# Performance work log

Hardware: AMD Instinct MI355X
Metric: run time of the kernel (lower is better)

## Reference

```python
import jax, jax.numpy as jnp
import numpy as np


def setup_inputs() -> dict:
    key = jax.random.key(0)
    kq, kk, kv, km = jax.random.split(key, 4)
    B, H, N, D = 2, 16, 2048, 64
    q = jax.random.normal(kq, (B, H, N, D), dtype=jnp.float32)
    k = jax.random.normal(kk, (B, H, N, D), dtype=jnp.float32)
    v = jax.random.normal(kv, (B, H, N, D), dtype=jnp.float32)
    # mask > 0 means position is masked OUT (matches torch masked_fill(mask > 0, -max))
    mask = jax.random.randint(km, (B, N), 0, 2, dtype=jnp.int32)
    return {"q": q, "k": k, "v": v, "mask": mask}


def reference(q, k, v, mask):
    # q,k,v: [b,h,n,d]; mask: [b,j] with >0 = masked
    scale = q.shape[-1] ** -0.5
    sim = jnp.einsum('bhid,bhjd->bhij', q, k) * scale
    # l2_dist score modification: 2*qk*scale - ||q||^2 - ||k||^2
    q_sq = jnp.sum(q * q, axis=-1, keepdims=True)          # [b,h,i,1]
    k_sq = jnp.sum(k * k, axis=-1, keepdims=True)          # [b,h,j,1]
    sim = sim * 2 - q_sq - jnp.swapaxes(k_sq, -1, -2)       # [b,h,i,j]
    neg_max = -jnp.finfo(sim.dtype).max
    m = (mask > 0)[:, None, None, :]                        # [b,1,1,j]
    sim = jnp.where(m, neg_max, sim)
    attn = jax.nn.softmax(sim, axis=-1)
    out = jnp.einsum('bhij,bhjd->bhid', attn, v)
    return out
```

## Files before the change

### kernel.cpp

```cpp
#include <hip/hip_runtime.h>
#include <hip/hip_bf16.h>

#define NSEQ 2048
#define DD   64
#define HH   16
#define QT   128
#define KVB  64
#define NKV  (NSEQ / KVB)

typedef __attribute__((ext_vector_type(4)))  float f4;
typedef __attribute__((ext_vector_type(16))) float f32x16;
typedef __attribute__((ext_vector_type(8)))  short bf16x8;
typedef __attribute__((ext_vector_type(4)))  unsigned int u32x4;
typedef __attribute__((ext_vector_type(2)))  unsigned int u32x2;

#define QSCL  0.36067376022224085f
#define LOG2E 1.4426950408889634f
#define NEGBIG (-1.0e30f)
#define THR   8.0f

#define SWZ(row, q)  (((row) << 6) + ((((q) ^ ((row) & 7))) << 3))
#define SWZV(d, q)   (((d) << 6) + ((((q) ^ (((d) >> 2) & 7) ^ ((d) & 3))) << 3))

#if defined(__has_builtin)
#if __has_builtin(__builtin_amdgcn_exp2f)
#define EXP2F __builtin_amdgcn_exp2f
#endif
#if __has_builtin(__builtin_amdgcn_permlane32_swap)
#define HAVE_PLSWAP 1
#endif
#endif
#ifndef EXP2F
#define EXP2F exp2f
#endif

union bfu { u32x4 u; bf16x8 h; };

__device__ __forceinline__ unsigned cvtpk(float lo, float hi) {
    unsigned r;
    asm("v_cvt_pk_bf16_f32 %0, %1, %2" : "=v"(r) : "v"(lo), "v"(hi));
    return r;
}
template<int CTRL>
__device__ __forceinline__ float dppf(float x) {
    return __int_as_float(__builtin_amdgcn_update_dpp(
        0, __float_as_int(x), CTRL, 0xF, 0xF, true));
}
__device__ __forceinline__ float cross_max(float x) {
#ifdef HAVE_PLSWAP
    u32x2 r = __builtin_amdgcn_permlane32_swap(__float_as_uint(x), __float_as_uint(x),
                                               false, false);
    return fmaxf(__uint_as_float(r[0]), __uint_as_float(r[1]));
#else
    return fmaxf(x, __shfl_xor(x, 32));
#endif
}
__device__ __forceinline__ float cross_add(float x) {
#ifdef HAVE_PLSWAP
    u32x2 r = __builtin_amdgcn_permlane32_swap(__float_as_uint(x), __float_as_uint(x),
                                               false, false);
    return __uint_as_float(r[0]) + __uint_as_float(r[1]);
#else
    return x + __shfl_xor(x, 32);
#endif
}

__global__ __launch_bounds__(256, 2)
void attend_kernel(const float* __restrict__ qg, const float* __restrict__ kg,
                   const float* __restrict__ vg, const int* __restrict__ maskg,
                   float* __restrict__ outg)
{
    __shared__ __align__(16) unsigned short Ks[2][KVB * DD];
    __shared__ __align__(16) unsigned short Vt[2][DD * KVB];
    __shared__ __align__(16) float bias_s[2][KVB];

    const int t    = threadIdx.x;
    const int w    = t >> 6;
    const int lane = t & 63;
    const int c5   = lane & 31;
    const int g2   = lane >> 5;

    const int p     = blockIdx.x;
    const int bh    = (p & 7) * 4 + ((p >> 3) >> 4);
    const int qtile = (p >> 3) & 15;
    const int b     = bh >> 4;

    const size_t base = (size_t)bh * NSEQ * DD;
    const float* kp = kg + base;
    const float* vp = vg + base;
    const int*   mp = maskg + b * NSEQ;

    bfu qf[4];
    {
        const float* qp = qg + base + (size_t)(qtile*QT + w*32 + c5) * DD;
        #pragma unroll
        for (int ck = 0; ck < 4; ++ck) {
            f4 a  = *(const f4*)(qp + ck*16 + g2*8);
            f4 bb = *(const f4*)(qp + ck*16 + g2*8 + 4);
            qf[ck].u = (u32x4){ cvtpk(a[0]*QSCL,  a[1]*QSCL),  cvtpk(a[2]*QSCL,  a[3]*QSCL),
                                cvtpk(bb[0]*QSCL, bb[1]*QSCL), cvtpk(bb[2]*QSCL, bb[3]*QSCL) };
        }
    }

    f32x16 acc0, acc1;
    #pragma unroll
    for (int r = 0; r < 16; ++r) { acc0[r] = 0.f; acc1[r] = 0.f; }
    float m_run = NEGBIG, l_run = 0.f;

    const bool isK = (w < 2);
    const int  jK  = t >> 1;
    const int  kq0 = (t & 1) * 4;
    const int  uv  = t & 127;
    const int  dq  = uv & 15;
    const int  jq  = uv >> 4;

    f4  st[8];
    int mr = 0;

    auto loadTile = [&](int gt) {
        const int j0 = gt * KVB;
        if (isK) {
            const float* src = kp + (size_t)(j0 + jK) * DD + kq0 * 8;
            #pragma unroll
            for (int i2 = 0; i2 < 8; ++i2) st[i2] = ((const f4*)src)[i2];
            mr = mp[j0 + jK];
        } else {
            #pragma unroll
            for (int i2 = 0; i2 < 8; ++i2)
                st[i2] = *(const f4*)(vp + (size_t)(j0 + jq*8 + i2) * DD + dq*4);
        }
    };

    auto stageTile = [&](int bsel) {
        if (isK) {
            float sq = 0.f;
            #pragma unroll
            for (int i2 = 0; i2 < 8; ++i2)
                sq += st[i2][0]*st[i2][0] + st[i2][1]*st[i2][1]
                    + st[i2][2]*st[i2][2] + st[i2][3]*st[i2][3];
            sq += dppf<0xB1>(sq);
            if ((t & 1) == 0) bias_s[bsel][jK] = (mr > 0) ? NEGBIG : -sq * LOG2E;
            #pragma unroll
            for (int s2 = 0; s2 < 4; ++s2) {
                u32x4 kk = (u32x4){ cvtpk(st[2*s2][0],   st[2*s2][1]),
                                    cvtpk(st[2*s2][2],   st[2*s2][3]),
                                    cvtpk(st[2*s2+1][0], st[2*s2+1][1]),
                                    cvtpk(st[2*s2+1][2], st[2*s2+1][3]) };
                *(u32x4*)&Ks[bsel][SWZ(jK, kq0 + s2)] = kk;
            }
        } else {
            #pragma unroll
            for (int cc = 0; cc < 4; ++cc) {
                int d = dq*4 + cc;
                u32x4 tv = (u32x4){ cvtpk(st[0][cc], st[1][cc]),
                                    cvtpk(st[2][cc], st[3][cc]),
                                    cvtpk(st[4][cc], st[5][cc]),
                                    cvtpk(st[6][cc], st[7][cc]) };
                *(u32x4*)&Vt[bsel][SWZV(d, jq)] = tv;
            }
        }
    };

    loadTile(0);
    stageTile(0);
    loadTile(1);
    __syncthreads();

    int cur = 0;
    for (int kt = 0; kt < NKV; ++kt) {
        if (kt + 1 < NKV) stageTile(cur ^ 1);
        if (kt + 2 < NKV) loadTile(kt + 2);

        f32x16 s01[2];
        #pragma unroll
        for (int jt = 0; jt < 2; ++jt) {
            f4 b4[4];
            #pragma unroll
            for (int q = 0; q < 4; ++q)
                b4[q] = *(const f4*)&bias_s[cur][32*jt + 8*q + 4*g2];
            f32x16 sc;
            #pragma unroll
            for (int r = 0; r < 16; ++r) sc[r] = b4[r>>2][r&3];
            __builtin_amdgcn_s_setprio(1);
            #pragma unroll
            for (int ck = 0; ck < 4; ++ck) {
                bfu kb;
                kb.u = *(const u32x4*)&Ks[cur][SWZ(32*jt + c5, 2*ck + g2)];
                sc = __builtin_amdgcn_mfma_f32_32x32x16_bf16(kb.h, qf[ck].h, sc, 0, 0, 0);
            }
            __builtin_amdgcn_s_setprio(0);
            s01[jt] = sc;
        }

        float pmax;
        {
            float mm[8];
            #pragma unroll
            for (int i2 = 0; i2 < 8; ++i2)
                mm[i2] = fmaxf(fmaxf(s01[0][2*i2], s01[0][2*i2+1]),
                               fmaxf(s01[1][2*i2], s01[1][2*i2+1]));
            float ma = fmaxf(fmaxf(mm[0], mm[1]), fmaxf(mm[2], mm[3]));
            float mb = fmaxf(fmaxf(mm[4], mm[5]), fmaxf(mm[6], mm[7]));
            pmax = fmaxf(ma, mb);
        }
        pmax = cross_max(pmax);
        if (!__all(pmax <= m_run + THR)) {
            float mn = fmaxf(m_run, pmax);
            float corr = EXP2F(m_run - mn);
            m_run = mn;
            l_run *= corr;
            #pragma unroll
            for (int r = 0; r < 16; ++r) { acc0[r] *= corr; acc1[r] *= corr; }
        }

        unsigned Wp[16];
        float ls0 = 0.f, ls1 = 0.f;
        #pragma unroll
        for (int jt = 0; jt < 2; ++jt) {
            #pragma unroll
            for (int m = 0; m < 8; ++m) {
                float e0 = EXP2F(s01[jt][2*m]   - m_run);
                float e1 = EXP2F(s01[jt][2*m+1] - m_run);
                if (m & 1) ls1 += e0 + e1; else ls0 += e0 + e1;
                Wp[jt*8 + m] = cvtpk(e0, e1);
            }
        }
        l_run += cross_add(ls0 + ls1);

        const bool hi = (g2 != 0);
        __builtin_amdgcn_s_setprio(1);
        #pragma unroll
        for (int ck = 0; ck < 4; ++ck) {
            const int bs = (ck >> 1) * 8 + 4 * (ck & 1);
            unsigned wA0 = Wp[bs], wA1 = Wp[bs+1], wB0 = Wp[bs+2], wB1 = Wp[bs+3];
            unsigned v  = hi ? wA0 : wB0;
            unsigned v2 = hi ? wA1 : wB1;
            unsigned x  = (unsigned)__shfl_xor((int)v, 32);
            unsigned x2 = (unsigned)__shfl_xor((int)v2, 32);
            bfu pb;
            pb.u = (u32x4){ hi ? x : wA0, hi ? x2 : wA1, hi ? wB0 : x, hi ? wB1 : x2 };
            bfu va0, va1;
            va0.u = *(const u32x4*)&Vt[cur][SWZV(     c5, 2*ck + g2)];
            va1.u = *(const u32x4*)&Vt[cur][SWZV(32 + c5, 2*ck + g2)];
            acc0 = __builtin_amdgcn_mfma_f32_32x32x16_bf16(va0.h, pb.h, acc0, 0, 0, 0);
            acc1 = __builtin_amdgcn_mfma_f32_32x32x16_bf16(va1.h, pb.h, acc1, 0, 0, 0);
        }
        __builtin_amdgcn_s_setprio(0);

        __syncthreads();
        cur ^= 1;
    }

    float inv = 1.0f / l_run;
    float* op = outg + base + (size_t)(qtile*QT + w*32 + c5) * DD;
    #pragma unroll
    for (int dt = 0; dt < 2; ++dt) {
        const f32x16 A = dt ? acc1 : acc0;
        #pragma unroll
        for (int q = 0; q < 4; ++q) {
            f4 o = { A[4*q]*inv, A[4*q+1]*inv, A[4*q+2]*inv, A[4*q+3]*inv };
            *(f4*)(op + 32*dt + 8*q + 4*g2) = o;
        }
    }
}

extern "C" void kernel_launch(void* const* d_in, const int* in_sizes, int n_in,
                              void* d_out, int out_size, void* d_ws, size_t ws_size,
                              hipStream_t stream) {
    const float* q    = (const float*)d_in[0];
    const float* k    = (const float*)d_in[1];
    const float* v    = (const float*)d_in[2];
    const int*   mask = (const int*)d_in[3];
    float* out = (float*)d_out;
    attend_kernel<<<dim3(512), dim3(256), 0, stream>>>(q, k, v, mask, out);
}
```

Measured before the change: 66.12 us.

## Split KV sequence across two wave groups per block and merge softmax partials

Doubles the block to 512 threads: two groups of four waves each handle alternating KV tiles (even/odd) for the same 128 query rows, with separate double-buffered K/V/bias shared memory per group. At the end the groups exchange running max and sum through shared memory, and one group writes its rescaled accumulators into reused K shared memory so the other can combine and store the output. This halves the serial KV loop length per wave and doubles waves per CU, in exchange for more shared memory, a final cross-group reduction and possible occupancy limits from launch_bounds(512,2).

```diff
diff --git a/kernel.cpp b/kernel.cpp
--- a/kernel.cpp
+++ b/kernel.cpp
@@ -7,6 +7,7 @@
 #define QT   128
 #define KVB  64
 #define NKV  (NSEQ / KVB)
+#define NR   (NKV / 2)
 
 typedef __attribute__((ext_vector_type(4)))  float f4;
 typedef __attribute__((ext_vector_type(16))) float f32x16;
@@ -65,20 +66,23 @@
 #endif
 }
 
-__global__ __launch_bounds__(256, 2)
+__global__ __launch_bounds__(512, 2)
 void attend_kernel(const float* __restrict__ qg, const float* __restrict__ kg,
                    const float* __restrict__ vg, const int* __restrict__ maskg,
                    float* __restrict__ outg)
 {
-    __shared__ __align__(16) unsigned short Ks[2][KVB * DD];
-    __shared__ __align__(16) unsigned short Vt[2][DD * KVB];
-    __shared__ __align__(16) float bias_s[2][KVB];
+    __shared__ __align__(16) unsigned short Ks[2][2][KVB * DD];
+    __shared__ __align__(16) unsigned short Vt[2][2][KVB * DD];
+    __shared__ __align__(16) float bias_s[2][2][KVB];
+    __shared__ __align__(16) float cmb_ml[2][4][64][2];
 
     const int t    = threadIdx.x;
     const int w    = t >> 6;
     const int lane = t & 63;
     const int c5   = lane & 31;
     const int g2   = lane >> 5;
+    const int g    = w >> 2;
+    const int rb   = w & 3;
 
     const int p     = blockIdx.x;
     const int bh    = (p & 7) * 4 + ((p >> 3) >> 4);
@@ -92,7 +96,7 @@
 
     bfu qf[4];
     {
-        const float* qp = qg + base + (size_t)(qtile*QT + w*32 + c5) * DD;
+        const float* qp = qg + base + (size_t)(qtile*QT + rb*32 + c5) * DD;
         #pragma unroll
         for (int ck = 0; ck < 4; ++ck) {
             f4 a  = *(const f4*)(qp + ck*16 + g2*8);
@@ -107,18 +111,20 @@
     for (int r = 0; r < 16; ++r) { acc0[r] = 0.f; acc1[r] = 0.f; }
     float m_run = NEGBIG, l_run = 0.f;
 
-    const bool isK = (w < 2);
-    const int  jK  = t >> 1;
-    const int  kq0 = (t & 1) * 4;
-    const int  uv  = t & 127;
-    const int  dq  = uv & 15;
-    const int  jq  = uv >> 4;
+    const int  srole = t >> 7;
+    const int  sid   = t & 127;
+    const int  spar  = srole >> 1;
+    const bool isK   = !(srole & 1);
+    const int  jK    = sid >> 1;
+    const int  kq0   = (sid & 1) * 4;
+    const int  dq    = sid & 15;
+    const int  jq    = sid >> 4;
 
     f4  st[8];
     int mr = 0;
 
-    auto loadTile = [&](int gt) {
-        const int j0 = gt * KVB;
+    auto loadTile = [&](int rr) {
+        const int j0 = (2*rr + spar) * KVB;
         if (isK) {
             const float* src = kp + (size_t)(j0 + jK) * DD + kq0 * 8;
             #pragma unroll
@@ -139,14 +145,14 @@
                 sq += st[i2][0]*st[i2][0] + st[i2][1]*st[i2][1]
                     + st[i2][2]*st[i2][2] + st[i2][3]*st[i2][3];
             sq += dppf<0xB1>(sq);
-            if ((t & 1) == 0) bias_s[bsel][jK] = (mr > 0) ? NEGBIG : -sq * LOG2E;
+            if ((sid & 1) == 0) bias_s[spar][bsel][jK] = (mr > 0) ? NEGBIG : -sq * LOG2E;
             #pragma unroll
             for (int s2 = 0; s2 < 4; ++s2) {
                 u32x4 kk = (u32x4){ cvtpk(st[2*s2][0],   st[2*s2][1]),
                                     cvtpk(st[2*s2][2],   st[2*s2][3]),
                                     cvtpk(st[2*s2+1][0], st[2*s2+1][1]),
                                     cvtpk(st[2*s2+1][2], st[2*s2+1][3]) };
-                *(u32x4*)&Ks[bsel][SWZ(jK, kq0 + s2)] = kk;
+                *(u32x4*)&Ks[spar][bsel][SWZ(jK, kq0 + s2)] = kk;
             }
         } else {
             #pragma unroll
@@ -156,7 +162,7 @@
                                     cvtpk(st[2][cc], st[3][cc]),
                                     cvtpk(st[4][cc], st[5][cc]),
                                     cvtpk(st[6][cc], st[7][cc]) };
-                *(u32x4*)&Vt[bsel][SWZV(d, jq)] = tv;
+                *(u32x4*)&Vt[spar][bsel][SWZV(d, jq)] = tv;
             }
         }
     };
@@ -166,10 +172,10 @@
     loadTile(1);
     __syncthreads();
 
-    int cur = 0;
-    for (int kt = 0; kt < NKV; ++kt) {
-        if (kt + 1 < NKV) stageTile(cur ^ 1);
-        if (kt + 2 < NKV) loadTile(kt + 2);
+    for (int r = 0; r < NR; ++r) {
+        const int cur = r & 1;
+        if (r + 1 < NR) stageTile(cur ^ 1);
+        if (r + 2 < NR) loadTile(r + 2);
 
         f32x16 s01[2];
         #pragma unroll
@@ -177,15 +183,15 @@
             f4 b4[4];
             #pragma unroll
             for (int q = 0; q < 4; ++q)
-                b4[q] = *(const f4*)&bias_s[cur][32*jt + 8*q + 4*g2];
+                b4[q] = *(const f4*)&bias_s[g][cur][32*jt + 8*q + 4*g2];
             f32x16 sc;
             #pragma unroll
-            for (int r = 0; r < 16; ++r) sc[r] = b4[r>>2][r&3];
+            for (int rr = 0; rr < 16; ++rr) sc[rr] = b4[rr>>2][rr&3];
             __builtin_amdgcn_s_setprio(1);
             #pragma unroll
             for (int ck = 0; ck < 4; ++ck) {
                 bfu kb;
-                kb.u = *(const u32x4*)&Ks[cur][SWZ(32*jt + c5, 2*ck + g2)];
+                kb.u = *(const u32x4*)&Ks[g][cur][SWZ(32*jt + c5, 2*ck + g2)];
                 sc = __builtin_amdgcn_mfma_f32_32x32x16_bf16(kb.h, qf[ck].h, sc, 0, 0, 0);
             }
             __builtin_amdgcn_s_setprio(0);
@@ -210,7 +216,7 @@
             m_run = mn;
             l_run *= corr;
             #pragma unroll
-            for (int r = 0; r < 16; ++r) { acc0[r] *= corr; acc1[r] *= corr; }
+            for (int rr = 0; rr < 16; ++rr) { acc0[rr] *= corr; acc1[rr] *= corr; }
         }
 
         unsigned Wp[16];
@@ -240,26 +246,49 @@
             bfu pb;
             pb.u = (u32x4){ hi ? x : wA0, hi ? x2 : wA1, hi ? wB0 : x, hi ? wB1 : x2 };
             bfu va0, va1;
-            va0.u = *(const u32x4*)&Vt[cur][SWZV(     c5, 2*ck + g2)];
-            va1.u = *(const u32x4*)&Vt[cur][SWZV(32 + c5, 2*ck + g2)];
+            va0.u = *(const u32x4*)&Vt[g][cur][SWZV(     c5, 2*ck + g2)];
+            va1.u = *(const u32x4*)&Vt[g][cur][SWZV(32 + c5, 2*ck + g2)];
             acc0 = __builtin_amdgcn_mfma_f32_32x32x16_bf16(va0.h, pb.h, acc0, 0, 0, 0);
             acc1 = __builtin_amdgcn_mfma_f32_32x32x16_bf16(va1.h, pb.h, acc1, 0, 0, 0);
         }
         __builtin_amdgcn_s_setprio(0);
 
         __syncthreads();
-        cur ^= 1;
     }
 
-    float inv = 1.0f / l_run;
-    float* op = outg + base + (size_t)(qtile*QT + w*32 + c5) * DD;
-    #pragma unroll
-    for (int dt = 0; dt < 2; ++dt) {
-        const f32x16 A = dt ? acc1 : acc0;
-        #pragma unroll
-        for (int q = 0; q < 4; ++q) {
-            f4 o = { A[4*q]*inv, A[4*q+1]*inv, A[4*q+2]*inv, A[4*q+3]*inv };
-            *(f4*)(op + 32*dt + 8*q + 4*g2) = o;
+    cmb_ml[g][rb][lane][0] = m_run;
+    cmb_ml[g][rb][lane][1] = l_run;
+    __syncthreads();
+    const float m_o = cmb_ml[g ^ 1][rb][lane][0];
+    const float l_o = cmb_ml[g ^ 1][rb][lane][1];
+    const float m_c  = fmaxf(m_run, m_o);
+    const float corr = EXP2F(m_run - m_c);
+    const float l_c  = l_run * corr + l_o * EXP2F(m_o - m_c);
+
+    float* X = (float*)&Ks[0][0][0];
+    if (g == 1) {
+        #pragma unroll
+        for (int q = 0; q < 16; ++q) X[(q      )*256 + rb*64 + lane] = acc0[q] * corr;
+        #pragma unroll
+        for (int q = 0; q < 16; ++q) X[(16 + q )*256 + rb*64 + lane] = acc1[q] * corr;
+    }
+    __syncthreads();
+    if (g == 0) {
+        const float inv = 1.0f / l_c;
+        float* op = outg + base + (size_t)(qtile*QT + rb*32 + c5) * DD;
+        #pragma unroll
+        for (int dt = 0; dt < 2; ++dt) {
+            const f32x16 A = dt ? acc1 : acc0;
+            #pragma unroll
+            for (int q = 0; q < 4; ++q) {
+                f4 o;
+                #pragma unroll
+                for (int e = 0; e < 4; ++e) {
+                    const int j = 4*q + e;
+                    o[e] = (A[j] * corr + X[(dt*16 + j)*256 + rb*64 + lane]) * inv;
+                }
+                *(f4*)(op + 32*dt + 8*q + 4*g2) = o;
+            }
         }
     }
 }
@@ -272,5 +301,5 @@
     const float* v    = (const float*)d_in[2];
     const int*   mask = (const int*)d_in[3];
     float* out = (float*)d_out;
-    attend_kernel<<<dim3(512), dim3(256), 0, stream>>>(q, k, v, mask, out);
-}
+    attend_kernel<<<dim3(512), dim3(512), 0, stream>>>(q, k, v, mask, out);
+}
```

Result: slower. 76.28 us (+15.4%).
